# Kernel tuning notes

Measured on AMD Instinct MI355X. Metric: run time of the kernel, lower is better.

The kernel has to match this reference:

```python
import jax, jax.numpy as jnp
import numpy as np

INPUT_DIM = 400
G_DIM = 3 * INPUT_DIM          # 1200, per-mention repr dim
GIJ_DIM = 9 * INPUT_DIM        # 3600, pair repr dim
HIDDEN = 150
M = 10000                      # candidate mentions
P = 2000                       # pruned mentions


def _pair_positions(P, K):
    """Static (numpy) construction of (i_pos, j_pos) into pruned_idx, matching
    the original double loop: for idx, for j in pruned_idx[max(0, idx-K):idx]."""
    I = np.repeat(np.arange(P)[:, None], K, axis=1)      # [P, K]
    Jpos = I - np.arange(K, 0, -1)[None, :]              # j = idx-K .. idx-1 (ascending)
    valid = Jpos >= 0
    return I[valid], Jpos[valid]                         # row-major => same ordering as loop


def setup_inputs() -> dict:
    key = jax.random.key(0)
    ks = jax.random.split(key, 8)
    mention_reprs = jax.random.normal(ks[0], (M, G_DIM), dtype=jnp.float32)
    pruned_idx = jnp.sort(jax.random.randint(ks[1], (P,), 0, M))
    s = 0.02
    return {
        "mention_reprs": mention_reprs,
        "pruned_idx": pruned_idx,
        "K": 50,
        "W1": jax.random.normal(ks[2], (GIJ_DIM, HIDDEN), dtype=jnp.float32) * s,
        "b1": jnp.zeros((HIDDEN,), dtype=jnp.float32),
        "W2": jax.random.normal(ks[3], (HIDDEN, HIDDEN), dtype=jnp.float32) * s,
        "b2": jnp.zeros((HIDDEN,), dtype=jnp.float32),
        "W3": jax.random.normal(ks[4], (HIDDEN, 1), dtype=jnp.float32) * s,
        "b3": jnp.zeros((1,), dtype=jnp.float32),
    }


def reference(mention_reprs, pruned_idx, K, W1, b1, W2, b2, W3, b3):
    P_ = pruned_idx.shape[0]
    i_pos, j_pos = _pair_positions(P_, int(K))           # static shapes
    g_i = mention_reprs[pruned_idx[i_pos]]               # [NP, G_DIM]
    g_j = mention_reprs[pruned_idx[j_pos]]               # [NP, G_DIM]
    pairwise = jnp.concatenate([g_i, g_j, g_i * g_j], axis=1)  # [NP, 9*input_dim]
    h = jax.nn.relu(pairwise @ W1 + b1)
    h = jax.nn.relu(h @ W2 + b2)
    return (h @ W3 + b3).squeeze(-1)                     # [NP]
```

## Files before the change

### kernel.cpp

```cpp
#include <hip/hip_runtime.h>
#include <hip/hip_bf16.h>


typedef __attribute__((ext_vector_type(8))) short short8;
typedef __attribute__((ext_vector_type(4))) float f32x4;

constexpr int DP    = 1216;
constexpr int HPAD  = 160;
constexpr int NKC   = 38;
constexpr int NKC2  = 5;
constexpr int WCH1  = 5120;
constexpr int KD    = 50;
constexpr int TI    = 5;
constexpr int PB    = TI * KD;
constexpr int NGR   = KD + TI;
constexpr int TD    = KD * (KD - 1) / 2;

__device__ __forceinline__ ushort bf16_rne(float x) {
  uint u = __float_as_uint(x);
  u += 0x7FFFu + ((u >> 16) & 1u);
  return (ushort)(u >> 16);
}
__device__ __forceinline__ float bf16f(ushort h) {
  return __uint_as_float((uint)h << 16);
}
__device__ __forceinline__ f32x4 mfma16(short8 a, short8 b, f32x4 c) {
  return __builtin_amdgcn_mfma_f32_16x16x32_bf16(a, b, c, 0, 0, 0);
}
__device__ __forceinline__ void g2lds16(const void* g, void* l) {
  __builtin_amdgcn_global_load_lds(
      (const __attribute__((address_space(1))) void*)g,
      (__attribute__((address_space(3))) void*)l, 16, 0, 0);
}
__device__ __forceinline__ void stage_hi(const ushort* gs, ushort* lb,
                                         int w, int lane) {
  const char* g = (const char*)gs + w * 1024 + lane * 16;
  char* l = (char*)lb + w * 1024;
  g2lds16(g, l);
  g2lds16(g + 4096, l + 4096);
  if (w < 2) g2lds16(g + 8192, l + 8192);
}
__device__ __forceinline__ void stage_G5(const float* __restrict__ G, int b0,
                                         int c, float* buf, int w, int lane) {
#pragma unroll
  for (int r = 0; r < 2; ++r) {
    const int slot = r * 256 + w * 64 + lane;
    int row = slot >> 3, grp = slot & 7;
    row = min(row, NGR - 1);
    const float* src =
        G + (size_t)(b0 + row) * DP + c * 32 + ((grp ^ (row & 7)) << 2);
    g2lds16(src, (char*)buf + (r * 256 + w * 64) * 16);
  }
}
__device__ __forceinline__ short8 mulcvt8(float4 a0, float4 a1, float4 b0,
                                          float4 b1) {
  float p[8] = {a0.x * b0.x, a0.y * b0.y, a0.z * b0.z, a0.w * b0.w,
                a1.x * b1.x, a1.y * b1.y, a1.z * b1.z, a1.w * b1.w};
  uint r[4];
#pragma unroll
  for (int e = 0; e < 4; ++e) {
    __hip_bfloat162 t = __float22bfloat162_rn(make_float2(p[2 * e], p[2 * e + 1]));
    r[e] = *(uint*)&t;
  }
  uint4 h = make_uint4(r[0], r[1], r[2], r[3]);
  return *(short8*)&h;
}
__device__ __forceinline__ void split1(const float* a, short8& hi, short8& lo) {
  const float4 a0 = *(const float4*)a, a1 = *(const float4*)(a + 4);
  float p[8] = {a0.x, a0.y, a0.z, a0.w, a1.x, a1.y, a1.z, a1.w};
  uint h[4], l[4];
#pragma unroll
  for (int e = 0; e < 4; ++e) {
    uint u0 = __float_as_uint(p[2 * e]), u1 = __float_as_uint(p[2 * e + 1]);
    float r0 = p[2 * e] - __uint_as_float(u0 & 0xffff0000u);
    float r1 = p[2 * e + 1] - __uint_as_float(u1 & 0xffff0000u);
    h[e] = __builtin_amdgcn_perm(u1, u0, 0x07060302u);
    l[e] = __builtin_amdgcn_perm(__float_as_uint(r1), __float_as_uint(r0),
                                 0x07060302u);
  }
  uint4 hu = make_uint4(h[0], h[1], h[2], h[3]);
  uint4 lu = make_uint4(l[0], l[1], l[2], l[3]);
  hi = *(short8*)&hu; lo = *(short8*)&lu;
}
__device__ __forceinline__ void pair_ij(int r, int K, int NP, int& i, int& j) {
  if (r >= NP) { i = 1; j = 0; return; }
  const int T = K * (K - 1) / 2;
  if (r < T) {
    int ii = (int)((1.0f + sqrtf(1.0f + 8.0f * (float)r)) * 0.5f);
    while (ii * (ii - 1) / 2 > r) --ii;
    while ((ii + 1) * ii / 2 <= r) ++ii;
    i = ii; j = r - ii * (ii - 1) / 2;
  } else {
    const int rp = r - T, q = rp / K;
    i = K + q; j = i - K + (rp - q * K);
  }
}

__global__ void k_prep_gather(const float* __restrict__ W1,
                              const float* __restrict__ W2,
                              const float* __restrict__ M,
                              const int* __restrict__ pidx,
                              ushort* __restrict__ W1ab_hi,
                              ushort* __restrict__ W1c_hi,
                              ushort* __restrict__ W2_hi,
                              float* __restrict__ G, int P) {
  if ((int)blockIdx.x < P) {
    const int i = blockIdx.x;
    const int r = pidx[i];
    const float4* src = reinterpret_cast<const float4*>(M + (size_t)r * 1200);
    float4* dst = reinterpret_cast<float4*>(G + (size_t)i * DP);
    for (int t = threadIdx.x; t < DP / 4; t += blockDim.x)
      dst[t] = (t < 300) ? src[t] : make_float4(0.f, 0.f, 0.f, 0.f);
    return;
  }
  const int NAB = 2 * NKC * HPAD * 32;
  const int NC = NKC * HPAD * 32;
  int idx = (blockIdx.x - P) * 256 + threadIdx.x;
  if (idx < NAB) {
    int s = idx / NC, r1 = idx % NC;
    int c = r1 / (HPAD * 32), r2 = r1 % (HPAD * 32);
    int col = r2 >> 5, kk = r2 & 31;
    int k = c * 32 + kk;
    float v = (k < 1200 && col < 150) ? W1[((size_t)s * 1200 + k) * 150 + col] : 0.f;
    int i0 = (col * 32 + kk) ^ ((col & 7) << 3);
    W1ab_hi[(size_t)(s * NKC + c) * WCH1 + i0] = bf16_rne(v);
  } else if (idx < NAB + NC) {
    int r1 = idx - NAB;
    int c = r1 / (HPAD * 32), r2 = r1 % (HPAD * 32);
    int col = r2 >> 5, kk = r2 & 31;
    int k = c * 32 + kk;
    float v = (k < 1200 && col < 150)
                  ? W1[((size_t)2 * 1200 + k) * 150 + col] : 0.f;
    int i0 = (col * 32 + kk) ^ ((col & 7) << 3);
    W1c_hi[(size_t)c * WCH1 + i0] = bf16_rne(v);
  } else {
    int r1 = idx - NAB - NC;
    if (r1 < NKC2 * HPAD * 32) {
      int c = r1 / (HPAD * 32), r2 = r1 % (HPAD * 32);
      int col = r2 >> 5, kk = r2 & 31;
      int k = c * 32 + kk;
      float v = (k < 150 && col < 150) ? W2[(size_t)k * 150 + col] : 0.f;
      int i0 = (col * 32 + kk) ^ ((col & 7) << 3);
      W2_hi[(size_t)c * WCH1 + i0] = bf16_rne(v);
    }
  }
}

__global__ __launch_bounds__(256, 4) void k_precomp(
    const float* __restrict__ G, const ushort* __restrict__ W1ab_hi,
    const float* __restrict__ b1, float* __restrict__ AB, int P) {
  __shared__ __align__(16) ushort Wb[2][WCH1];
  const int tid = threadIdx.x, lane = tid & 63, w = tid >> 6;
  const int l15 = lane & 15, kb = lane >> 4;
  const int rt = w & 1, ch = w >> 1;
  const int r0 = blockIdx.x * 32;
  const int slab = blockIdx.y;
  const ushort* wsrc = W1ab_hi + (size_t)slab * NKC * WCH1;

  const int row = min(r0 + rt * 16 + l15, P - 1);
  const float* g = G + (size_t)row * DP + kb * 8;
  const int lbase = (l15 * 32 + kb * 8) ^ ((l15 & 7) << 3);

  f32x4 acc[5];
#pragma unroll
  for (int b = 0; b < 5; ++b) acc[b] = (f32x4)(0.f);

  stage_hi(wsrc, Wb[0], w, lane);
  short8 ah, al;
  split1(g, ah, al);

  for (int c = 0; c < NKC; ++c) {
    __syncthreads();
    if (c < NKC - 1)
      stage_hi(wsrc + (size_t)(c + 1) * WCH1, Wb[(c + 1) & 1], w, lane);
    const ushort* wb = Wb[c & 1];
#pragma unroll
    for (int ct = 0; ct < 5; ++ct) {
      const short8 bh = *(const short8*)&wb[(ch * 5 + ct) * 512 + lbase];
      acc[ct] = mfma16(ah, bh, acc[ct]);
      acc[ct] = mfma16(al, bh, acc[ct]);
    }
    if (c < NKC - 1) split1(g + (c + 1) * 32, ah, al);
  }
  float* outp = AB + (size_t)slab * P * HPAD;
#pragma unroll
  for (int q = 0; q < 4; ++q) {
    const int r = r0 + rt * 16 + kb * 4 + q;
    if (r < P) {
#pragma unroll
      for (int ct = 0; ct < 5; ++ct) {
        const int col = (ch * 5 + ct) * 16 + l15;
        float v = acc[ct][q];
        if (slab == 0 && col < 150) v += b1[col];
        outp[(size_t)r * HPAD + col] = v;
      }
    }
  }
}

__global__ __launch_bounds__(256, 2) void k_pair(
    const float* __restrict__ G, const ushort* __restrict__ W1c_hi,
    const ushort* __restrict__ W2_hi, const float* __restrict__ AB,
    const float* __restrict__ b2, const float* __restrict__ W3,
    const float* __restrict__ b3, ushort* __restrict__ H1,
    float* __restrict__ out, int P, int K, int NP, int ND, int wlimHead) {
  __shared__ __align__(16) char smem[38912];
  ushort* Wb0 = (ushort*)smem;
  ushort* Wb1 = (ushort*)(smem + 10240);
  float*  Gs0 = (float*)(smem + 20480);
  float*  Gs1 = (float*)(smem + 28672);
  int* tI = (int*)(smem + 36864);
  int* tJ = (int*)(smem + 37888);

  const int tid = threadIdx.x, lane = tid & 63, w = tid >> 6;
  const int l15 = lane & 15, kb = lane >> 4;
  const int lswz = (l15 * 32 + kb * 8) ^ ((l15 & 7) << 3);
  const float* ABB = AB + (size_t)P * HPAD;

  if ((int)blockIdx.x < ND) {
    const int q8 = ND >> 3, r8 = ND & 7;
    const int xcd = blockIdx.x & 7, sidx = blockIdx.x >> 3;
    const int bid = (xcd < r8) ? xcd * (q8 + 1) + sidx
                               : r8 * (q8 + 1) + (xcd - r8) * q8 + sidx;
    const int i0 = KD + bid * TI;
    const int b0 = i0 - KD;
    ushort* H1blk = H1 + (size_t)(TD + (size_t)bid * PB) * HPAD;

    uint sI[4], sJ[4];
#pragma unroll
    for (int rt = 0; rt < 4; ++rt) {
      const int q = min(w * 64 + rt * 16 + l15, PB - 1);
      const int li = KD + q / KD, lj = q / KD + q % KD;
      sI[rt] = li * 8 + ((2 * kb) ^ (li & 7));
      sJ[rt] = lj * 8 + ((2 * kb) ^ (lj & 7));
    }

    {
      f32x4 acc[4][10];
#pragma unroll
      for (int a = 0; a < 4; ++a)
#pragma unroll
        for (int b = 0; b < 10; ++b) acc[a][b] = (f32x4)(0.f);

      stage_G5(G, b0, 0, Gs0, w, lane);
      stage_hi(W1c_hi, Wb0, w, lane);
      __syncthreads();

#pragma unroll 2
      for (int c = 0; c < NKC; ++c) {
        if (c) __syncthreads();
        if (c < NKC - 1) {
          stage_G5(G, b0, c + 1, (c & 1) ? Gs0 : Gs1, w, lane);
          stage_hi(W1c_hi + (size_t)(c + 1) * WCH1, (c & 1) ? Wb0 : Wb1, w, lane);
        }
        const float4* gp = (const float4*)((c & 1) ? Gs1 : Gs0);
        const ushort* wb = (c & 1) ? Wb1 : Wb0;
        short8 a[4];
#pragma unroll
        for (int rt = 0; rt < 4; ++rt)
          a[rt] = mulcvt8(gp[sI[rt]], gp[sI[rt] ^ 1], gp[sJ[rt]], gp[sJ[rt] ^ 1]);
#pragma unroll
        for (int ct = 0; ct < 10; ++ct) {
          const short8 bh = *(const short8*)&wb[ct * 512 + lswz];
          acc[0][ct] = mfma16(a[0], bh, acc[0][ct]);
          acc[1][ct] = mfma16(a[1], bh, acc[1][ct]);
          acc[2][ct] = mfma16(a[2], bh, acc[2][ct]);
          acc[3][ct] = mfma16(a[3], bh, acc[3][ct]);
        }
      }

#pragma unroll
      for (int rt = 0; rt < 4; ++rt)
#pragma unroll
        for (int qq = 0; qq < 4; ++qq) {
          const int rr = w * 64 + rt * 16 + kb * 4 + qq;
          if (rr < PB) {
            const int ii = i0 + rr / KD;
            const int jj = ii - KD + rr % KD;
            const float* Ar = AB + (size_t)ii * HPAD;
            const float* Br = ABB + (size_t)jj * HPAD;
            ushort* hrow = H1blk + (size_t)rr * HPAD;
#pragma unroll
            for (int ct = 0; ct < 10; ++ct) {
              const int col = ct * 16 + l15;
              const float v = acc[rt][ct][qq] + Ar[col] + Br[col];
              hrow[col] = bf16_rne(fmaxf(v, 0.f));
            }
          }
        }
    }

    asm volatile("s_waitcnt vmcnt(0)" ::: "memory");
    const ushort* h1p[4];
#pragma unroll
    for (int rt = 0; rt < 4; ++rt) {
      const int rr = min(w * 64 + rt * 16 + l15, PB - 1);
      h1p[rt] = H1blk + (size_t)rr * HPAD + kb * 8;
    }
    float b2v[10], w3v[10];
#pragma unroll
    for (int ct = 0; ct < 10; ++ct) {
      const int col = ct * 16 + l15;
      b2v[ct] = (col < 150) ? b2[col] : 0.f;
      w3v[ct] = (col < 150) ? W3[col] : 0.f;
    }
    const float b3v = b3[0];

    f32x4 acc2[4][10];
#pragma unroll
    for (int a = 0; a < 4; ++a)
#pragma unroll
      for (int b = 0; b < 10; ++b) acc2[a][b] = (f32x4)(0.f);

    stage_hi(W2_hi, Wb0, w, lane);
    short8 a2[4];
#pragma unroll
    for (int rt = 0; rt < 4; ++rt) a2[rt] = *(const short8*)h1p[rt];

#pragma unroll
    for (int c2 = 0; c2 < NKC2; ++c2) {
      __syncthreads();
      if (c2 < NKC2 - 1)
        stage_hi(W2_hi + (size_t)(c2 + 1) * WCH1, (c2 & 1) ? Wb0 : Wb1, w, lane);
      const ushort* wb = (c2 & 1) ? Wb1 : Wb0;
#pragma unroll
      for (int ct = 0; ct < 10; ++ct) {
        const short8 bh = *(const short8*)&wb[ct * 512 + lswz];
        acc2[0][ct] = mfma16(a2[0], bh, acc2[0][ct]);
        acc2[1][ct] = mfma16(a2[1], bh, acc2[1][ct]);
        acc2[2][ct] = mfma16(a2[2], bh, acc2[2][ct]);
        acc2[3][ct] = mfma16(a2[3], bh, acc2[3][ct]);
      }
      if (c2 < NKC2 - 1) {
#pragma unroll
        for (int rt = 0; rt < 4; ++rt)
          a2[rt] = *(const short8*)(h1p[rt] + (c2 + 1) * 32);
      }
    }
#pragma unroll
    for (int rt = 0; rt < 4; ++rt)
#pragma unroll
      for (int qq = 0; qq < 4; ++qq) {
        float s = 0.f;
#pragma unroll
        for (int ct = 0; ct < 10; ++ct)
          s = fmaf(fmaxf(acc2[rt][ct][qq] + b2v[ct], 0.f), w3v[ct], s);
        s += __shfl_xor(s, 1); s += __shfl_xor(s, 2);
        s += __shfl_xor(s, 4); s += __shfl_xor(s, 8);
        if (l15 == 0) {
          const int rr = w * 64 + rt * 16 + kb * 4 + qq;
          if (rr < PB) out[TD + (size_t)bid * PB + rr] = s + b3v;
        }
      }
  } else {
    const int r0 = ((int)blockIdx.x - ND) * 128;
    const int wlim = wlimHead;
    if (tid < 128) {
      int i, j;
      pair_ij(r0 + tid, K, NP, i, j);
      tI[tid] = i; tJ[tid] = j;
    }
    stage_hi(W1c_hi, Wb0, w, lane);
    __syncthreads();

    const int rowA = w * 32 + l15, rowB = rowA + 16;
    const float* gi0 = G + (size_t)tI[rowA] * DP + kb * 8;
    const float* gj0 = G + (size_t)tJ[rowA] * DP + kb * 8;
    const float* gi1 = G + (size_t)tI[rowB] * DP + kb * 8;
    const float* gj1 = G + (size_t)tJ[rowB] * DP + kb * 8;

    {
      f32x4 acc[2][10];
#pragma unroll
      for (int a = 0; a < 2; ++a)
#pragma unroll
        for (int b = 0; b < 10; ++b) acc[a][b] = (f32x4)(0.f);

      float4 x00 = *(const float4*)gi0, x01 = *(const float4*)(gi0 + 4);
      float4 y00 = *(const float4*)gj0, y01 = *(const float4*)(gj0 + 4);
      float4 x10 = *(const float4*)gi1, x11 = *(const float4*)(gi1 + 4);
      float4 y10 = *(const float4*)gj1, y11 = *(const float4*)(gj1 + 4);

#pragma unroll 2
      for (int c = 0; c < NKC; ++c) {
        if (c) __syncthreads();
        if (c < NKC - 1)
          stage_hi(W1c_hi + (size_t)(c + 1) * WCH1, (c & 1) ? Wb0 : Wb1, w, lane);
        const short8 a0 = mulcvt8(x00, x01, y00, y01);
        const short8 a1 = mulcvt8(x10, x11, y10, y11);
        if (c < NKC - 1) {
          const int cn = c + 1;
          x00 = *(const float4*)(gi0 + cn * 32); x01 = *(const float4*)(gi0 + cn * 32 + 4);
          y00 = *(const float4*)(gj0 + cn * 32); y01 = *(const float4*)(gj0 + cn * 32 + 4);
          x10 = *(const float4*)(gi1 + cn * 32); x11 = *(const float4*)(gi1 + cn * 32 + 4);
          y10 = *(const float4*)(gj1 + cn * 32); y11 = *(const float4*)(gj1 + cn * 32 + 4);
        }
        const ushort* wb = (c & 1) ? Wb1 : Wb0;
#pragma unroll
        for (int ct = 0; ct < 10; ++ct) {
          const short8 bh = *(const short8*)&wb[ct * 512 + lswz];
          acc[0][ct] = mfma16(a0, bh, acc[0][ct]);
          acc[1][ct] = mfma16(a1, bh, acc[1][ct]);
        }
      }

#pragma unroll
      for (int rt = 0; rt < 2; ++rt)
#pragma unroll
        for (int qq = 0; qq < 4; ++qq) {
          const int rr = w * 32 + rt * 16 + kb * 4 + qq;
          const int gr = r0 + rr;
          if (gr < wlim) {
            const float* Ar = AB + (size_t)tI[rr] * HPAD;
            const float* Br = ABB + (size_t)tJ[rr] * HPAD;
            ushort* hrow = H1 + (size_t)gr * HPAD;
#pragma unroll
            for (int ct = 0; ct < 10; ++ct) {
              const int col = ct * 16 + l15;
              const float v = acc[rt][ct][qq] + Ar[col] + Br[col];
              hrow[col] = bf16_rne(fmaxf(v, 0.f));
            }
          }
        }
    }

    asm volatile("s_waitcnt vmcnt(0)" ::: "memory");
    const ushort* h1p[2];
#pragma unroll
    for (int rt = 0; rt < 2; ++rt) {
      const int gr = min(r0 + w * 32 + rt * 16 + l15, NP - 1);
      h1p[rt] = H1 + (size_t)gr * HPAD + kb * 8;
    }
    float b2v[10], w3v[10];
#pragma unroll
    for (int ct = 0; ct < 10; ++ct) {
      const int col = ct * 16 + l15;
      b2v[ct] = (col < 150) ? b2[col] : 0.f;
      w3v[ct] = (col < 150) ? W3[col] : 0.f;
    }
    const float b3v = b3[0];

    f32x4 acc2[2][10];
#pragma unroll
    for (int a = 0; a < 2; ++a)
#pragma unroll
      for (int b = 0; b < 10; ++b) acc2[a][b] = (f32x4)(0.f);

    stage_hi(W2_hi, Wb0, w, lane);
    short8 a2[2];
#pragma unroll
    for (int rt = 0; rt < 2; ++rt) a2[rt] = *(const short8*)h1p[rt];

#pragma unroll
    for (int c2 = 0; c2 < NKC2; ++c2) {
      __syncthreads();
      if (c2 < NKC2 - 1)
        stage_hi(W2_hi + (size_t)(c2 + 1) * WCH1, (c2 & 1) ? Wb0 : Wb1, w, lane);
      const ushort* wb = (c2 & 1) ? Wb1 : Wb0;
#pragma unroll
      for (int ct = 0; ct < 10; ++ct) {
        const short8 bh = *(const short8*)&wb[ct * 512 + lswz];
        acc2[0][ct] = mfma16(a2[0], bh, acc2[0][ct]);
        acc2[1][ct] = mfma16(a2[1], bh, acc2[1][ct]);
      }
      if (c2 < NKC2 - 1) {
#pragma unroll
        for (int rt = 0; rt < 2; ++rt)
          a2[rt] = *(const short8*)(h1p[rt] + (c2 + 1) * 32);
      }
    }
#pragma unroll
    for (int rt = 0; rt < 2; ++rt)
#pragma unroll
      for (int qq = 0; qq < 4; ++qq) {
        float s = 0.f;
#pragma unroll
        for (int ct = 0; ct < 10; ++ct)
          s = fmaf(fmaxf(acc2[rt][ct][qq] + b2v[ct], 0.f), w3v[ct], s);
        s += __shfl_xor(s, 1); s += __shfl_xor(s, 2);
        s += __shfl_xor(s, 4); s += __shfl_xor(s, 8);
        if (l15 == 0) {
          const int gr = r0 + w * 32 + rt * 16 + kb * 4 + qq;
          if (gr < wlim) out[gr] = s + b3v;
        }
      }
  }
}

extern "C" void kernel_launch(void* const* d_in, const int* in_sizes, int n_in,
                              void* d_out, int out_size, void* d_ws, size_t ws_size,
                              hipStream_t stream) {
  const float* M    = (const float*)d_in[0];
  const int*   pidx = (const int*)d_in[1];
  const float* W1   = (const float*)d_in[3];
  const float* b1   = (const float*)d_in[4];
  const float* W2   = (const float*)d_in[5];
  const float* b2   = (const float*)d_in[6];
  const float* W3   = (const float*)d_in[7];
  const float* b3   = (const float*)d_in[8];
  float* out = (float*)d_out;

  const int P = in_sizes[1];
  const int NP = out_size;
  int K = 50;
  for (int k = 1; k <= P; ++k) {
    const long long np = (long long)k * (k - 1) / 2 + (long long)(P - k) * k;
    if (np == (long long)NP) { K = k; break; }
  }

  float* G = (float*)d_ws;
  float* AB = G + (size_t)P * DP;
  ushort* W1ab_hi = (ushort*)(AB + (size_t)2 * P * HPAD);
  ushort* W1c_hi = W1ab_hi + (size_t)2 * NKC * WCH1;
  ushort* W2_hi = W1c_hi + (size_t)NKC * WCH1;
  ushort* H1 = W2_hi + (size_t)NKC2 * WCH1;

  const int prepN = (2 * NKC + NKC + NKC2) * HPAD * 32;
  const int prepB = (prepN + 255) / 256;
  k_prep_gather<<<P + prepB, 256, 0, stream>>>(W1, W2, M, pidx, W1ab_hi,
                                               W1c_hi, W2_hi, G, P);
  dim3 gp((P + 31) / 32, 2);
  k_precomp<<<gp, 256, 0, stream>>>(G, W1ab_hi, b1, AB, P);

  int ND = 0, wlimHead, headB;
  if (K == KD && P > KD && (P - KD) % TI == 0) {
    ND = (P - KD) / TI;
    wlimHead = TD;
    headB = (TD + 127) / 128;
  } else {
    wlimHead = NP;
    headB = (NP + 127) / 128;
  }
  k_pair<<<ND + headB, 256, 0, stream>>>(G, W1c_hi, W2_hi, AB, b2, W3, b3, H1,
                                         out, P, K, NP, ND, wlimHead);
}
```

Baseline: 116.9 us.

## Stage 128-wide K phases in k_pair to cut barrier count

The pair kernel's K loop now stages four 32-wide chunks (128 elements) of W1c and G per phase into a much larger LDS buffer (~140KB), so there are 10 phases and barriers instead of 38. G row pitch and the W1c image are padded to 1280/40 chunks to match, and launch bounds drop to one block per SM. The aim is less synchronisation overhead and longer compute per staged batch, at the cost of occupancy and more padding work.

Result: slower. 169.3 us (+44.8%).

```diff
diff --git a/kernel.cpp b/kernel.cpp
--- a/kernel.cpp
+++ b/kernel.cpp
@@ -5,9 +5,11 @@
 typedef __attribute__((ext_vector_type(8))) short short8;
 typedef __attribute__((ext_vector_type(4))) float f32x4;
 
-constexpr int DP    = 1216;
+constexpr int DP    = 1280;
 constexpr int HPAD  = 160;
-constexpr int NKC   = 38;
+constexpr int NPH   = 10;
+constexpr int NKCP  = 38;
+constexpr int NIMG  = 40;
 constexpr int NKC2  = 5;
 constexpr int WCH1  = 5120;
 constexpr int KD    = 50;
@@ -16,6 +18,14 @@
 constexpr int NGR   = KD + TI;
 constexpr int TD    = KD * (KD - 1) / 2;
 
+constexpr int OFF_WB0 = 0;
+constexpr int OFF_WB1 = 40960;
+constexpr int OFF_GS0 = 81920;
+constexpr int OFF_GS1 = 110592;
+constexpr int OFF_TI  = 139264;
+constexpr int OFF_TJ  = 139776;
+constexpr int SMEM_SZ = 140288;
+
 __device__ __forceinline__ ushort bf16_rne(float x) {
   uint u = __float_as_uint(x);
   u += 0x7FFFu + ((u >> 16) & 1u);
@@ -31,6 +41,13 @@
   __builtin_amdgcn_global_load_lds(
       (const __attribute__((address_space(1))) void*)g,
       (__attribute__((address_space(3))) void*)l, 16, 0, 0);
+}
+__device__ __forceinline__ void stage_W128(const ushort* gs, ushort* lb,
+                                           int w, int lane) {
+  const char* g = (const char*)gs + w * 1024 + lane * 16;
+  char* l = (char*)lb + w * 1024;
+#pragma unroll
+  for (int r = 0; r < 10; ++r) g2lds16(g + r * 4096, l + r * 4096);
 }
 __device__ __forceinline__ void stage_hi(const ushort* gs, ushort* lb,
                                          int w, int lane) {
@@ -40,16 +57,16 @@
   g2lds16(g + 4096, l + 4096);
   if (w < 2) g2lds16(g + 8192, l + 8192);
 }
-__device__ __forceinline__ void stage_G5(const float* __restrict__ G, int b0,
-                                         int c, float* buf, int w, int lane) {
-#pragma unroll
-  for (int r = 0; r < 2; ++r) {
+__device__ __forceinline__ void stage_G128(const float* __restrict__ G, int b0,
+                                           int c, float* buf, int w, int lane) {
+#pragma unroll
+  for (int r = 0; r < 7; ++r) {
     const int slot = r * 256 + w * 64 + lane;
-    int row = slot >> 3, grp = slot & 7;
+    int row = slot >> 5, g5 = slot & 31;
     row = min(row, NGR - 1);
-    const float* src =
-        G + (size_t)(b0 + row) * DP + c * 32 + ((grp ^ (row & 7)) << 2);
-    g2lds16(src, (char*)buf + (r * 256 + w * 64) * 16);
+    const float* src = G + (size_t)(b0 + row) * DP + c * 128 +
+                       (((g5 & 24) | ((g5 & 7) ^ (row & 7))) << 2);
+    g2lds16(src, (char*)buf + slot * 16);
   }
 }
 __device__ __forceinline__ short8 mulcvt8(float4 a0, float4 a1, float4 b0,
@@ -113,17 +130,17 @@
       dst[t] = (t < 300) ? src[t] : make_float4(0.f, 0.f, 0.f, 0.f);
     return;
   }
-  const int NAB = 2 * NKC * HPAD * 32;
-  const int NC = NKC * HPAD * 32;
+  const int NAB = 2 * NKCP * HPAD * 32;
+  const int NC = NIMG * HPAD * 32;
   int idx = (blockIdx.x - P) * 256 + threadIdx.x;
   if (idx < NAB) {
-    int s = idx / NC, r1 = idx % NC;
+    int s = idx / (NKCP * HPAD * 32), r1 = idx % (NKCP * HPAD * 32);
     int c = r1 / (HPAD * 32), r2 = r1 % (HPAD * 32);
     int col = r2 >> 5, kk = r2 & 31;
     int k = c * 32 + kk;
     float v = (k < 1200 && col < 150) ? W1[((size_t)s * 1200 + k) * 150 + col] : 0.f;
     int i0 = (col * 32 + kk) ^ ((col & 7) << 3);
-    W1ab_hi[(size_t)(s * NKC + c) * WCH1 + i0] = bf16_rne(v);
+    W1ab_hi[(size_t)(s * NKCP + c) * WCH1 + i0] = bf16_rne(v);
   } else if (idx < NAB + NC) {
     int r1 = idx - NAB;
     int c = r1 / (HPAD * 32), r2 = r1 % (HPAD * 32);
@@ -155,7 +172,7 @@
   const int rt = w & 1, ch = w >> 1;
   const int r0 = blockIdx.x * 32;
   const int slab = blockIdx.y;
-  const ushort* wsrc = W1ab_hi + (size_t)slab * NKC * WCH1;
+  const ushort* wsrc = W1ab_hi + (size_t)slab * NKCP * WCH1;
 
   const int row = min(r0 + rt * 16 + l15, P - 1);
   const float* g = G + (size_t)row * DP + kb * 8;
@@ -169,9 +186,9 @@
   short8 ah, al;
   split1(g, ah, al);
 
-  for (int c = 0; c < NKC; ++c) {
+  for (int c = 0; c < NKCP; ++c) {
     __syncthreads();
-    if (c < NKC - 1)
+    if (c < NKCP - 1)
       stage_hi(wsrc + (size_t)(c + 1) * WCH1, Wb[(c + 1) & 1], w, lane);
     const ushort* wb = Wb[c & 1];
 #pragma unroll
@@ -180,7 +197,7 @@
       acc[ct] = mfma16(ah, bh, acc[ct]);
       acc[ct] = mfma16(al, bh, acc[ct]);
     }
-    if (c < NKC - 1) split1(g + (c + 1) * 32, ah, al);
+    if (c < NKCP - 1) split1(g + (c + 1) * 32, ah, al);
   }
   float* outp = AB + (size_t)slab * P * HPAD;
 #pragma unroll
@@ -198,19 +215,19 @@
   }
 }
 
-__global__ __launch_bounds__(256, 2) void k_pair(
+__global__ __launch_bounds__(256, 1) void k_pair(
     const float* __restrict__ G, const ushort* __restrict__ W1c_hi,
     const ushort* __restrict__ W2_hi, const float* __restrict__ AB,
     const float* __restrict__ b2, const float* __restrict__ W3,
     const float* __restrict__ b3, ushort* __restrict__ H1,
     float* __restrict__ out, int P, int K, int NP, int ND, int wlimHead) {
-  __shared__ __align__(16) char smem[38912];
-  ushort* Wb0 = (ushort*)smem;
-  ushort* Wb1 = (ushort*)(smem + 10240);
-  float*  Gs0 = (float*)(smem + 20480);
-  float*  Gs1 = (float*)(smem + 28672);
-  int* tI = (int*)(smem + 36864);
-  int* tJ = (int*)(smem + 37888);
+  __shared__ __align__(16) char smem[SMEM_SZ];
+  ushort* Wb0 = (ushort*)(smem + OFF_WB0);
+  ushort* Wb1 = (ushort*)(smem + OFF_WB1);
+  float*  Gs0 = (float*)(smem + OFF_GS0);
+  float*  Gs1 = (float*)(smem + OFF_GS1);
+  int* tI = (int*)(smem + OFF_TI);
+  int* tJ = (int*)(smem + OFF_TJ);
 
   const int tid = threadIdx.x, lane = tid & 63, w = tid >> 6;
   const int l15 = lane & 15, kb = lane >> 4;
@@ -231,8 +248,8 @@
     for (int rt = 0; rt < 4; ++rt) {
       const int q = min(w * 64 + rt * 16 + l15, PB - 1);
       const int li = KD + q / KD, lj = q / KD + q % KD;
-      sI[rt] = li * 8 + ((2 * kb) ^ (li & 7));
-      sJ[rt] = lj * 8 + ((2 * kb) ^ (lj & 7));
+      sI[rt] = li * 32 + ((2 * kb) ^ (li & 7));
+      sJ[rt] = lj * 32 + ((2 * kb) ^ (lj & 7));
     }
 
     {
@@ -242,30 +259,36 @@
 #pragma unroll
         for (int b = 0; b < 10; ++b) acc[a][b] = (f32x4)(0.f);
 
-      stage_G5(G, b0, 0, Gs0, w, lane);
-      stage_hi(W1c_hi, Wb0, w, lane);
+      stage_G128(G, b0, 0, Gs0, w, lane);
+      stage_W128(W1c_hi, Wb0, w, lane);
       __syncthreads();
 
-#pragma unroll 2
-      for (int c = 0; c < NKC; ++c) {
+      for (int c = 0; c < NPH; ++c) {
         if (c) __syncthreads();
-        if (c < NKC - 1) {
-          stage_G5(G, b0, c + 1, (c & 1) ? Gs0 : Gs1, w, lane);
-          stage_hi(W1c_hi + (size_t)(c + 1) * WCH1, (c & 1) ? Wb0 : Wb1, w, lane);
+        if (c < NPH - 1) {
+          stage_G128(G, b0, c + 1, (c & 1) ? Gs0 : Gs1, w, lane);
+          stage_W128(W1c_hi + (size_t)(c + 1) * 4 * WCH1, (c & 1) ? Wb0 : Wb1,
+                     w, lane);
         }
         const float4* gp = (const float4*)((c & 1) ? Gs1 : Gs0);
         const ushort* wb = (c & 1) ? Wb1 : Wb0;
-        short8 a[4];
-#pragma unroll
-        for (int rt = 0; rt < 4; ++rt)
-          a[rt] = mulcvt8(gp[sI[rt]], gp[sI[rt] ^ 1], gp[sJ[rt]], gp[sJ[rt] ^ 1]);
-#pragma unroll
-        for (int ct = 0; ct < 10; ++ct) {
-          const short8 bh = *(const short8*)&wb[ct * 512 + lswz];
-          acc[0][ct] = mfma16(a[0], bh, acc[0][ct]);
-          acc[1][ct] = mfma16(a[1], bh, acc[1][ct]);
-          acc[2][ct] = mfma16(a[2], bh, acc[2][ct]);
-          acc[3][ct] = mfma16(a[3], bh, acc[3][ct]);
+#pragma unroll
+        for (int ks = 0; ks < 4; ++ks) {
+          short8 a[4];
+#pragma unroll
+          for (int rt = 0; rt < 4; ++rt) {
+            const uint si = sI[rt] + ks * 8, sj = sJ[rt] + ks * 8;
+            a[rt] = mulcvt8(gp[si], gp[si ^ 1], gp[sj], gp[sj ^ 1]);
+          }
+          const ushort* wks = wb + ks * WCH1;
+#pragma unroll
+          for (int ct = 0; ct < 10; ++ct) {
+            const short8 bh = *(const short8*)&wks[ct * 512 + lswz];
+            acc[0][ct] = mfma16(a[0], bh, acc[0][ct]);
+            acc[1][ct] = mfma16(a[1], bh, acc[1][ct]);
+            acc[2][ct] = mfma16(a[2], bh, acc[2][ct]);
+            acc[3][ct] = mfma16(a[3], bh, acc[3][ct]);
+          }
         }
       }
 
@@ -360,7 +383,7 @@
       pair_ij(r0 + tid, K, NP, i, j);
       tI[tid] = i; tJ[tid] = j;
     }
-    stage_hi(W1c_hi, Wb0, w, lane);
+    stage_W128(W1c_hi, Wb0, w, lane);
     __syncthreads();
 
     const int rowA = w * 32 + l15, rowB = rowA + 16;
@@ -376,31 +399,28 @@
 #pragma unroll
         for (int b = 0; b < 10; ++b) acc[a][b] = (f32x4)(0.f);
 
-      float4 x00 = *(const float4*)gi0, x01 = *(const float4*)(gi0 + 4);
-      float4 y00 = *(const float4*)gj0, y01 = *(const float4*)(gj0 + 4);
-      float4 x10 = *(const float4*)gi1, x11 = *(const float4*)(gi1 + 4);
-      float4 y10 = *(const float4*)gj1, y11 = *(const float4*)(gj1 + 4);
-
-#pragma unroll 2
-      for (int c = 0; c < NKC; ++c) {
+      for (int c = 0; c < NPH; ++c) {
         if (c) __syncthreads();
-        if (c < NKC - 1)
-          stage_hi(W1c_hi + (size_t)(c + 1) * WCH1, (c & 1) ? Wb0 : Wb1, w, lane);
-        const short8 a0 = mulcvt8(x00, x01, y00, y01);
-        const short8 a1 = mulcvt8(x10, x11, y10, y11);
-        if (c < NKC - 1) {
-          const int cn = c + 1;
-          x00 = *(const float4*)(gi0 + cn * 32); x01 = *(const float4*)(gi0 + cn * 32 + 4);
-          y00 = *(const float4*)(gj0 + cn * 32); y01 = *(const float4*)(gj0 + cn * 32 + 4);
-          x10 = *(const float4*)(gi1 + cn * 32); x11 = *(const float4*)(gi1 + cn * 32 + 4);
-          y10 = *(const float4*)(gj1 + cn * 32); y11 = *(const float4*)(gj1 + cn * 32 + 4);
-        }
+        if (c < NPH - 1)
+          stage_W128(W1c_hi + (size_t)(c + 1) * 4 * WCH1, (c & 1) ? Wb0 : Wb1,
+                     w, lane);
         const ushort* wb = (c & 1) ? Wb1 : Wb0;
 #pragma unroll
-        for (int ct = 0; ct < 10; ++ct) {
-          const short8 bh = *(const short8*)&wb[ct * 512 + lswz];
-          acc[0][ct] = mfma16(a0, bh, acc[0][ct]);
-          acc[1][ct] = mfma16(a1, bh, acc[1][ct]);
+        for (int ks = 0; ks < 4; ++ks) {
+          const int off = c * 128 + ks * 32;
+          const short8 a0 =
+              mulcvt8(*(const float4*)(gi0 + off), *(const float4*)(gi0 + off + 4),
+                      *(const float4*)(gj0 + off), *(const float4*)(gj0 + off + 4));
+          const short8 a1 =
+              mulcvt8(*(const float4*)(gi1 + off), *(const float4*)(gi1 + off + 4),
+                      *(const float4*)(gj1 + off), *(const float4*)(gj1 + off + 4));
+          const ushort* wks = wb + ks * WCH1;
+#pragma unroll
+          for (int ct = 0; ct < 10; ++ct) {
+            const short8 bh = *(const short8*)&wks[ct * 512 + lswz];
+            acc[0][ct] = mfma16(a0, bh, acc[0][ct]);
+            acc[1][ct] = mfma16(a1, bh, acc[1][ct]);
+          }
         }
       }
 
@@ -511,11 +531,11 @@
   float* G = (float*)d_ws;
   float* AB = G + (size_t)P * DP;
   ushort* W1ab_hi = (ushort*)(AB + (size_t)2 * P * HPAD);
-  ushort* W1c_hi = W1ab_hi + (size_t)2 * NKC * WCH1;
-  ushort* W2_hi = W1c_hi + (size_t)NKC * WCH1;
+  ushort* W1c_hi = W1ab_hi + (size_t)2 * NKCP * WCH1;
+  ushort* W2_hi = W1c_hi + (size_t)NIMG * WCH1;
   ushort* H1 = W2_hi + (size_t)NKC2 * WCH1;
 
-  const int prepN = (2 * NKC + NKC + NKC2) * HPAD * 32;
+  const int prepN = (2 * NKCP + NIMG + NKC2) * HPAD * 32;
   const int prepB = (prepN + 255) / 256;
   k_prep_gather<<<P + prepB, 256, 0, stream>>>(W1, W2, M, pidx, W1ab_hi,
                                                W1c_hi, W2_hi, G, P);
```

## Triple-buffer W1/G staging in dense pair path with explicit vmcnt waits

Applied to the files above, without the earlier changes.

Replaces the double-buffered LDS staging of G rows and W1 chunks in the dense block path with a three-stage ring, issuing loads two chunks ahead. Per-iteration __syncthreads is swapped for a partial s_waitcnt vmcnt plus a raw s_barrier, so loads for the next chunk can still be in flight while the current one is consumed. Shared memory grows from about 38 KB to 56 KB per block, which may limit occupancy under the 2-blocks-per-CU launch bound. The exact vmcnt counts must match the number of global-to-LDS loads each wave issues.

Measured after the change: 116.2 us. About the same (-0.6%).

```diff
diff --git a/kernel.cpp b/kernel.cpp
--- a/kernel.cpp
+++ b/kernel.cpp
@@ -16,6 +16,16 @@
 constexpr int NGR   = KD + TI;
 constexpr int TD    = KD * (KD - 1) / 2;
 
+constexpr int OFF_WQ0 = 0;
+constexpr int OFF_WQ1 = 10240;
+constexpr int OFF_WQ2 = 20480;
+constexpr int OFF_GQ0 = 30720;
+constexpr int OFF_GQ1 = 38912;
+constexpr int OFF_GQ2 = 47104;
+constexpr int OFF_TI  = 55296;
+constexpr int OFF_TJ  = 55808;
+constexpr int SMEM_SZ = 56320;
+
 __device__ __forceinline__ ushort bf16_rne(float x) {
   uint u = __float_as_uint(x);
   u += 0x7FFFu + ((u >> 16) & 1u);
@@ -40,7 +50,7 @@
   g2lds16(g + 4096, l + 4096);
   if (w < 2) g2lds16(g + 8192, l + 8192);
 }
-__device__ __forceinline__ void stage_G5(const float* __restrict__ G, int b0,
+__device__ __forceinline__ void stage_G5(const float* __restrict__ G, int gw0,
                                          int c, float* buf, int w, int lane) {
 #pragma unroll
   for (int r = 0; r < 2; ++r) {
@@ -48,7 +58,7 @@
     int row = slot >> 3, grp = slot & 7;
     row = min(row, NGR - 1);
     const float* src =
-        G + (size_t)(b0 + row) * DP + c * 32 + ((grp ^ (row & 7)) << 2);
+        G + (size_t)(gw0 + row) * DP + c * 32 + ((grp ^ (row & 7)) << 2);
     g2lds16(src, (char*)buf + (r * 256 + w * 64) * 16);
   }
 }
@@ -204,13 +214,15 @@
     const float* __restrict__ b2, const float* __restrict__ W3,
     const float* __restrict__ b3, ushort* __restrict__ H1,
     float* __restrict__ out, int P, int K, int NP, int ND, int wlimHead) {
-  __shared__ __align__(16) char smem[38912];
-  ushort* Wb0 = (ushort*)smem;
-  ushort* Wb1 = (ushort*)(smem + 10240);
-  float*  Gs0 = (float*)(smem + 20480);
-  float*  Gs1 = (float*)(smem + 28672);
-  int* tI = (int*)(smem + 36864);
-  int* tJ = (int*)(smem + 37888);
+  __shared__ __align__(16) char smem[SMEM_SZ];
+  ushort* Wq0 = (ushort*)(smem + OFF_WQ0);
+  ushort* Wq1 = (ushort*)(smem + OFF_WQ1);
+  ushort* Wq2 = (ushort*)(smem + OFF_WQ2);
+  float*  Gq0 = (float*)(smem + OFF_GQ0);
+  float*  Gq1 = (float*)(smem + OFF_GQ1);
+  float*  Gq2 = (float*)(smem + OFF_GQ2);
+  int* tI = (int*)(smem + OFF_TI);
+  int* tJ = (int*)(smem + OFF_TJ);
 
   const int tid = threadIdx.x, lane = tid & 63, w = tid >> 6;
   const int l15 = lane & 15, kb = lane >> 4;
@@ -223,7 +235,7 @@
     const int bid = (xcd < r8) ? xcd * (q8 + 1) + sidx
                                : r8 * (q8 + 1) + (xcd - r8) * q8 + sidx;
     const int i0 = KD + bid * TI;
-    const int b0 = i0 - KD;
+    const int gw0 = i0 - KD;
     ushort* H1blk = H1 + (size_t)(TD + (size_t)bid * PB) * HPAD;
 
     uint sI[4], sJ[4];
@@ -242,32 +254,54 @@
 #pragma unroll
         for (int b = 0; b < 10; ++b) acc[a][b] = (f32x4)(0.f);
 
-      stage_G5(G, b0, 0, Gs0, w, lane);
-      stage_hi(W1c_hi, Wb0, w, lane);
-      __syncthreads();
-
-#pragma unroll 2
-      for (int c = 0; c < NKC; ++c) {
-        if (c) __syncthreads();
-        if (c < NKC - 1) {
-          stage_G5(G, b0, c + 1, (c & 1) ? Gs0 : Gs1, w, lane);
-          stage_hi(W1c_hi + (size_t)(c + 1) * WCH1, (c & 1) ? Wb0 : Wb1, w, lane);
-        }
-        const float4* gp = (const float4*)((c & 1) ? Gs1 : Gs0);
-        const ushort* wb = (c & 1) ? Wb1 : Wb0;
-        short8 a[4];
-#pragma unroll
-        for (int rt = 0; rt < 4; ++rt)
-          a[rt] = mulcvt8(gp[sI[rt]], gp[sI[rt] ^ 1], gp[sJ[rt]], gp[sJ[rt] ^ 1]);
-#pragma unroll
-        for (int ct = 0; ct < 10; ++ct) {
-          const short8 bh = *(const short8*)&wb[ct * 512 + lswz];
-          acc[0][ct] = mfma16(a[0], bh, acc[0][ct]);
-          acc[1][ct] = mfma16(a[1], bh, acc[1][ct]);
-          acc[2][ct] = mfma16(a[2], bh, acc[2][ct]);
-          acc[3][ct] = mfma16(a[3], bh, acc[3][ct]);
-        }
-      }
+      stage_G5(G, gw0, 0, Gq0, w, lane);
+      stage_hi(W1c_hi, Wq0, w, lane);
+      stage_G5(G, gw0, 1, Gq1, w, lane);
+      stage_hi(W1c_hi + (size_t)1 * WCH1, Wq1, w, lane);
+      __builtin_amdgcn_sched_barrier(0);
+      asm volatile("s_waitcnt vmcnt(4)" ::: "memory");
+      __builtin_amdgcn_s_barrier();
+      __builtin_amdgcn_sched_barrier(0);
+
+#define D_ITER(CI, GCUR, WCUR, GN, WN, VM)                                     \
+  do {                                                                         \
+    if ((CI) + 2 < NKC) {                                                      \
+      stage_G5(G, gw0, (CI) + 2, (GN), w, lane);                               \
+      stage_hi(W1c_hi + (size_t)((CI) + 2) * WCH1, (WN), w, lane);             \
+    }                                                                          \
+    __builtin_amdgcn_sched_barrier(0);                                         \
+    asm volatile("s_waitcnt vmcnt(" #VM ")" ::: "memory");                     \
+    __builtin_amdgcn_sched_barrier(0);                                         \
+    {                                                                          \
+      const float4* gp_ = (const float4*)(GCUR);                               \
+      const ushort* wb_ = (WCUR);                                              \
+      short8 a_[4];                                                            \
+      _Pragma("unroll")                                                        \
+      for (int rt = 0; rt < 4; ++rt) {                                         \
+        const uint si = sI[rt], sj = sJ[rt];                                   \
+        a_[rt] = mulcvt8(gp_[si], gp_[si ^ 1], gp_[sj], gp_[sj ^ 1]);          \
+      }                                                                        \
+      _Pragma("unroll")                                                        \
+      for (int ct = 0; ct < 10; ++ct) {                                        \
+        const short8 bh = *(const short8*)&wb_[ct * 512 + lswz];               \
+        acc[0][ct] = mfma16(a_[0], bh, acc[0][ct]);                            \
+        acc[1][ct] = mfma16(a_[1], bh, acc[1][ct]);                            \
+        acc[2][ct] = mfma16(a_[2], bh, acc[2][ct]);                            \
+        acc[3][ct] = mfma16(a_[3], bh, acc[3][ct]);                            \
+      }                                                                        \
+    }                                                                          \
+    __builtin_amdgcn_s_barrier();                                              \
+  } while (0)
+
+      for (int t = 0; t < 12; ++t) {
+        const int c = t * 3;
+        D_ITER(c,     Gq0, Wq0, Gq2, Wq2, 4);
+        D_ITER(c + 1, Gq1, Wq1, Gq0, Wq0, 4);
+        D_ITER(c + 2, Gq2, Wq2, Gq1, Wq1, 4);
+      }
+      D_ITER(36, Gq0, Wq0, Gq2, Wq2, 0);
+      D_ITER(37, Gq1, Wq1, Gq2, Wq2, 0);
+#undef D_ITER
 
 #pragma unroll
       for (int rt = 0; rt < 4; ++rt)
@@ -312,7 +346,7 @@
 #pragma unroll
       for (int b = 0; b < 10; ++b) acc2[a][b] = (f32x4)(0.f);
 
-    stage_hi(W2_hi, Wb0, w, lane);
+    stage_hi(W2_hi, Wq0, w, lane);
     short8 a2[4];
 #pragma unroll
     for (int rt = 0; rt < 4; ++rt) a2[rt] = *(const short8*)h1p[rt];
@@ -321,8 +355,8 @@
     for (int c2 = 0; c2 < NKC2; ++c2) {
       __syncthreads();
       if (c2 < NKC2 - 1)
-        stage_hi(W2_hi + (size_t)(c2 + 1) * WCH1, (c2 & 1) ? Wb0 : Wb1, w, lane);
-      const ushort* wb = (c2 & 1) ? Wb1 : Wb0;
+        stage_hi(W2_hi + (size_t)(c2 + 1) * WCH1, (c2 & 1) ? Wq0 : Wq1, w, lane);
+      const ushort* wb = (c2 & 1) ? Wq1 : Wq0;
 #pragma unroll
       for (int ct = 0; ct < 10; ++ct) {
         const short8 bh = *(const short8*)&wb[ct * 512 + lswz];
@@ -360,7 +394,7 @@
       pair_ij(r0 + tid, K, NP, i, j);
       tI[tid] = i; tJ[tid] = j;
     }
-    stage_hi(W1c_hi, Wb0, w, lane);
+    stage_hi(W1c_hi, Wq0, w, lane);
     __syncthreads();
 
     const int rowA = w * 32 + l15, rowB = rowA + 16;
@@ -385,7 +419,7 @@
       for (int c = 0; c < NKC; ++c) {
         if (c) __syncthreads();
         if (c < NKC - 1)
-          stage_hi(W1c_hi + (size_t)(c + 1) * WCH1, (c & 1) ? Wb0 : Wb1, w, lane);
+          stage_hi(W1c_hi + (size_t)(c + 1) * WCH1, (c & 1) ? Wq0 : Wq1, w, lane);
         const short8 a0 = mulcvt8(x00, x01, y00, y01);
         const short8 a1 = mulcvt8(x10, x11, y10, y11);
         if (c < NKC - 1) {
@@ -395,7 +429,7 @@
           x10 = *(const float4*)(gi1 + cn * 32); x11 = *(const float4*)(gi1 + cn * 32 + 4);
           y10 = *(const float4*)(gj1 + cn * 32); y11 = *(const float4*)(gj1 + cn * 32 + 4);
         }
-        const ushort* wb = (c & 1) ? Wb1 : Wb0;
+        const ushort* wb = (c & 1) ? Wq1 : Wq0;
 #pragma unroll
         for (int ct = 0; ct < 10; ++ct) {
           const short8 bh = *(const short8*)&wb[ct * 512 + lswz];
@@ -446,7 +480,7 @@
 #pragma unroll
       for (int b = 0; b < 10; ++b) acc2[a][b] = (f32x4)(0.f);
 
-    stage_hi(W2_hi, Wb0, w, lane);
+    stage_hi(W2_hi, Wq0, w, lane);
     short8 a2[2];
 #pragma unroll
     for (int rt = 0; rt < 2; ++rt) a2[rt] = *(const short8*)h1p[rt];
@@ -455,8 +489,8 @@
     for (int c2 = 0; c2 < NKC2; ++c2) {
       __syncthreads();
       if (c2 < NKC2 - 1)
-        stage_hi(W2_hi + (size_t)(c2 + 1) * WCH1, (c2 & 1) ? Wb0 : Wb1, w, lane);
-      const ushort* wb = (c2 & 1) ? Wb1 : Wb0;
+        stage_hi(W2_hi + (size_t)(c2 + 1) * WCH1, (c2 & 1) ? Wq0 : Wq1, w, lane);
+      const ushort* wb = (c2 & 1) ? Wq1 : Wq0;
 #pragma unroll
       for (int ct = 0; ct < 10; ++ct) {
         const short8 bh = *(const short8*)&wb[ct * 512 + lswz];
```
